# Performance work log

Hardware: AMD Instinct MI355X
Metric: run time of the kernel (lower is better)

Reference implementation:

```python
import jax, jax.numpy as jnp
import numpy as np

NUM_HEADS = 8


def _conv1(x, w, b):
    # 1x1x1 Conv3d == per-voxel channel linear map. x: [B,C,D,H,W], w: [O,C], b: [O]
    return jnp.einsum('bcdhw,oc->bodhw', x, w) + b[None, :, None, None, None]


def setup_inputs() -> dict:
    key = jax.random.key(0)
    ks = jax.random.split(key, 7)
    B, C, D, H, W = 1, 64, 16, 16, 16
    s = 0.02
    return {
        'decoder_features': jax.random.normal(ks[0], (B, C, D, H, W), jnp.float32),
        'mae_features': jax.random.normal(ks[1], (B, C, D, H, W), jnp.float32),
        'q_w': jax.random.normal(ks[2], (C, C), jnp.float32) * s,
        'q_b': jnp.zeros((C,), jnp.float32),
        'k_w': jax.random.normal(ks[3], (C, C), jnp.float32) * s,
        'k_b': jnp.zeros((C,), jnp.float32),
        'v_w': jax.random.normal(ks[4], (C, C), jnp.float32) * s,
        'v_b': jnp.zeros((C,), jnp.float32),
        'o_w': jax.random.normal(ks[5], (C, C), jnp.float32) * s,
        'o_b': jnp.zeros((C,), jnp.float32),
    }


def reference(decoder_features, mae_features, q_w, q_b, k_w, k_b, v_w, v_b, o_w, o_b):
    B, C, D, H, W = decoder_features.shape
    nh = NUM_HEADS
    hd = C // nh
    N = D * H * W
    scale = hd ** -0.5

    def split_heads(x):
        # [B,C,D,H,W] -> [B, nh, N, hd]
        return x.reshape(B, nh, hd, N).transpose(0, 1, 3, 2)

    Q = split_heads(_conv1(decoder_features, q_w, q_b))
    K = split_heads(_conv1(mae_features, k_w, k_b))
    V = split_heads(_conv1(mae_features, v_w, v_b))

    attn = jax.nn.softmax(jnp.einsum('bhnc,bhmc->bhnm', Q, K) * scale, axis=-1)
    out = jnp.einsum('bhnm,bhmc->bhnc', attn, V)  # [B, nh, N, hd]
    out = out.transpose(0, 1, 3, 2).reshape(B, C, D, H, W)
    return _conv1(out, o_w, o_b)
```

## Files before the change

kernel.cpp:

```cpp
#include <hip/hip_runtime.h>
#include <hip/hip_bf16.h>
#include <math.h>


#define N_VOX 4096
#define NH 8
#define QSCALE 0.51010813f

typedef unsigned short ushort_t;
typedef __attribute__((ext_vector_type(8))) short bf16x8;
typedef __attribute__((ext_vector_type(16))) float f32x16;

__device__ __forceinline__ unsigned short f2bf(float f) {
  union { float f; unsigned u; } v; v.f = f;
  unsigned r = v.u + 0x7FFFu + ((v.u >> 16) & 1u);
  return (unsigned short)(r >> 16);
}
__device__ __forceinline__ unsigned pk2bf(float a, float b) {
  __hip_bfloat162 h = __float22bfloat162_rn(float2{a, b});
  union { __hip_bfloat162 h; unsigned u; } c; c.h = h;
  return c.u;
}
__device__ __forceinline__ float ex2(float x) { return __builtin_amdgcn_exp2f(x); }

__global__ __launch_bounds__(256) void qkv_pack(
    const float* __restrict__ dec, const float* __restrict__ mae,
    const float* __restrict__ qw, const float* __restrict__ qb_,
    const float* __restrict__ kw, const float* __restrict__ kb,
    const float* __restrict__ vw, const float* __restrict__ vb,
    ushort_t* __restrict__ Qp, ushort_t* __restrict__ Kp,
    ushort_t* __restrict__ Vt, ushort_t* __restrict__ zeroblk) {
  const int bx = blockIdx.x;
  const int n = blockIdx.y * 256 + threadIdx.x;

  if (bx < 8) {
    const int h = bx;
    float x[64];
#pragma unroll
    for (int c = 0; c < 64; ++c) x[c] = dec[c * N_VOX + n];
    float qv[8];
#pragma unroll
    for (int j = 0; j < 8; ++j) {
      const int o = h * 8 + j;
      float a = qb_[o];
#pragma unroll
      for (int c = 0; c < 64; ++c) a = fmaf(x[c], qw[o * 64 + c], a);
      qv[j] = a * QSCALE;
    }
    uint4 pk;
    pk.x = pk2bf(qv[0], qv[1]); pk.y = pk2bf(qv[2], qv[3]);
    pk.z = pk2bf(qv[4], qv[5]); pk.w = pk2bf(qv[6], qv[7]);
    *(uint4*)(Qp + ((size_t)h * N_VOX + n) * 8) = pk;
  } else {
    const int h = bx - 8;
    float x[64];
#pragma unroll
    for (int c = 0; c < 64; ++c) x[c] = mae[c * N_VOX + n];
    float kv[8], vv[8];
#pragma unroll
    for (int j = 0; j < 8; ++j) {
      const int o = h * 8 + j;
      float a = kb[o], b = vb[o];
#pragma unroll
      for (int c = 0; c < 64; ++c) {
        a = fmaf(x[c], kw[o * 64 + c], a);
        b = fmaf(x[c], vw[o * 64 + c], b);
      }
      kv[j] = a; vv[j] = b;
    }
    uint4 pk;
    pk.x = pk2bf(kv[0], kv[1]); pk.y = pk2bf(kv[2], kv[3]);
    pk.z = pk2bf(kv[4], kv[5]); pk.w = pk2bf(kv[6], kv[7]);
    *(uint4*)(Kp + ((size_t)h * N_VOX + n) * 8) = pk;
#pragma unroll
    for (int d = 0; d < 8; ++d)
      Vt[((size_t)(h * 32 + d)) * N_VOX + n] = f2bf(vv[d]);
    Vt[((size_t)(h * 32 + 8)) * N_VOX + n] = 0x3F80;
    if (h == 0 && n < 8) zeroblk[n] = 0;
  }
}

__global__ __launch_bounds__(256, 3) void attn_mfma(
    const ushort_t* __restrict__ Qp, const ushort_t* __restrict__ Kp,
    const ushort_t* __restrict__ Vt, const ushort_t* __restrict__ zeroblk,
    float* __restrict__ o_part, int kps) {
  const int tid = threadIdx.x;
  const int lane = tid & 63;
  const int wave = tid >> 6;
  const int l31 = lane & 31;
  const int lhalf = lane >> 5;
  const int h = blockIdx.y;
  const int ks = blockIdx.z;
  const int qb = blockIdx.x * 256 + wave * 64;

  __shared__ ushort_t P_lds[8][32 * 36];

  bf16x8 qfrag0 = *(const bf16x8*)(Qp + ((size_t)h * N_VOX + qb + l31) * 8);
  bf16x8 qfrag1 = *(const bf16x8*)(Qp + ((size_t)h * N_VOX + qb + 32 + l31) * 8);

  f32x16 zf, acc0, acc1;
#pragma unroll
  for (int i = 0; i < 16; ++i) { zf[i] = 0.f; acc0[i] = 0.f; acc1[i] = 0.f; }

  const ushort_t* KpH = Kp + (size_t)h * N_VOX * 8;
  const ushort_t* VtH = Vt + ((size_t)h * 32 + l31) * N_VOX;
  ushort_t* pb0 = &P_lds[wave * 2 + 0][l31 * 36];
  ushort_t* pb1 = &P_lds[wave * 2 + 1][l31 * 36];

  const int kbeg = ks * kps;
  for (int kk = 0; kk < kps; kk += 32) {
    const int kcur = kbeg + kk;
    const ushort_t* kp = lhalf ? zeroblk : (KpH + (size_t)(kcur + l31) * 8);
    bf16x8 kf = *(const bf16x8*)kp;

    f32x16 s0 = __builtin_amdgcn_mfma_f32_32x32x16_bf16(kf, qfrag0, zf, 0, 0, 0);
    f32x16 s1 = __builtin_amdgcn_mfma_f32_32x32x16_bf16(kf, qfrag1, zf, 0, 0, 0);

    bf16x8 vf0 = *(const bf16x8*)(VtH + kcur + lhalf * 8);
    bf16x8 vf1 = *(const bf16x8*)(VtH + kcur + 16 + lhalf * 8);

#pragma unroll
    for (int G = 0; G < 4; ++G) {
      uint2 w;
      w.x = pk2bf(ex2(s0[G * 4 + 0]), ex2(s0[G * 4 + 1]));
      w.y = pk2bf(ex2(s0[G * 4 + 2]), ex2(s0[G * 4 + 3]));
      *(uint2*)(pb0 + G * 8 + lhalf * 4) = w;
    }
#pragma unroll
    for (int G = 0; G < 4; ++G) {
      uint2 w;
      w.x = pk2bf(ex2(s1[G * 4 + 0]), ex2(s1[G * 4 + 1]));
      w.y = pk2bf(ex2(s1[G * 4 + 2]), ex2(s1[G * 4 + 3]));
      *(uint2*)(pb1 + G * 8 + lhalf * 4) = w;
    }

#pragma unroll
    for (int grp = 0; grp < 2; ++grp) {
      union { bf16x8 v; uint2 u[2]; } p0, p1;
      p0.u[0] = *(const uint2*)(pb0 + grp * 16 + lhalf * 8);
      p0.u[1] = *(const uint2*)(pb0 + grp * 16 + lhalf * 8 + 4);
      p1.u[0] = *(const uint2*)(pb1 + grp * 16 + lhalf * 8);
      p1.u[1] = *(const uint2*)(pb1 + grp * 16 + lhalf * 8 + 4);
      const bf16x8 vf = grp ? vf1 : vf0;
      acc0 = __builtin_amdgcn_mfma_f32_32x32x16_bf16(p0.v, vf, acc0, 0, 0, 0);
      acc1 = __builtin_amdgcn_mfma_f32_32x32x16_bf16(p1.v, vf, acc1, 0, 0, 0);
    }
  }

  if (l31 < 9) {
    float* ob = o_part + ((size_t)(ks * NH + h) * 9 + l31) * N_VOX;
#pragma unroll
    for (int t = 0; t < 2; ++t) {
      const f32x16 a = t ? acc1 : acc0;
      const int qst = qb + t * 32 + 4 * lhalf;
#pragma unroll
      for (int G = 0; G < 4; ++G) {
        float4 v4 = make_float4(a[G * 4 + 0], a[G * 4 + 1], a[G * 4 + 2], a[G * 4 + 3]);
        *(float4*)(ob + qst + 8 * G) = v4;
      }
    }
  }
}

__global__ __launch_bounds__(256) void combine(
    const float* __restrict__ o_part, float* __restrict__ ocomb, int KS) {
  const int t = blockIdx.x * 256 + threadIdx.x;
  const int c = t >> 12, n = t & (N_VOX - 1);
  const int h = c >> 3, d = c & 7;
  float so = 0.f, sl = 0.f;
  for (int s = 0; s < KS; ++s) {
    const float* base = o_part + ((size_t)(s * NH + h) * 9) * N_VOX;
    so += base[d * N_VOX + n];
    sl += base[8 * N_VOX + n];
  }
  ocomb[(size_t)c * N_VOX + n] = so / sl;
}

__global__ __launch_bounds__(256) void out_proj(
    const float* __restrict__ ocomb, const float* __restrict__ ow,
    const float* __restrict__ obias, float* __restrict__ out) {
  const int og = blockIdx.x;
  const int n = blockIdx.y * 256 + threadIdx.x;
  float x[64];
#pragma unroll
  for (int c = 0; c < 64; ++c) x[c] = ocomb[c * N_VOX + n];
#pragma unroll
  for (int j = 0; j < 8; ++j) {
    const int o = og * 8 + j;
    float acc = obias[o];
#pragma unroll
    for (int c = 0; c < 64; ++c) acc = fmaf(x[c], ow[o * 64 + c], acc);
    out[o * N_VOX + n] = acc;
  }
}

extern "C" void kernel_launch(void* const* d_in, const int* in_sizes, int n_in,
                              void* d_out, int out_size, void* d_ws, size_t ws_size,
                              hipStream_t stream) {
  const float* dec = (const float*)d_in[0];
  const float* mae = (const float*)d_in[1];
  const float* qw = (const float*)d_in[2];
  const float* qb = (const float*)d_in[3];
  const float* kw = (const float*)d_in[4];
  const float* kb = (const float*)d_in[5];
  const float* vw = (const float*)d_in[6];
  const float* vb = (const float*)d_in[7];
  const float* ow = (const float*)d_in[8];
  const float* ob = (const float*)d_in[9];
  float* out = (float*)d_out;
  char* ws = (char*)d_ws;

  const size_t OFF_QP = 0;
  const size_t OFF_KP = 0x80000;
  const size_t OFF_ZERO = 0x100000;
  const size_t OFF_VT = 0x101000;
  const size_t OFF_OPART = 0x301000;

  int KS = 8;
  while (KS > 1) {
    size_t need = OFF_OPART + (size_t)KS * NH * 9 * N_VOX * 4 + 64ull * N_VOX * 4;
    if (need <= ws_size) break;
    KS >>= 1;
  }
  const size_t OFF_OCOMB = OFF_OPART + (size_t)KS * NH * 9 * N_VOX * 4;

  ushort_t* Qp = (ushort_t*)(ws + OFF_QP);
  ushort_t* Kp = (ushort_t*)(ws + OFF_KP);
  ushort_t* zb = (ushort_t*)(ws + OFF_ZERO);
  ushort_t* Vt = (ushort_t*)(ws + OFF_VT);
  float* o_part = (float*)(ws + OFF_OPART);
  float* ocomb = (float*)(ws + OFF_OCOMB);

  qkv_pack<<<dim3(16, 16), 256, 0, stream>>>(dec, mae, qw, qb, kw, kb, vw, vb,
                                             Qp, Kp, Vt, zb);
  attn_mfma<<<dim3(16, 8, KS), 256, 0, stream>>>(Qp, Kp, Vt, zb, o_part,
                                                 N_VOX / KS);
  combine<<<1024, 256, 0, stream>>>(o_part, ocomb, KS);
  out_proj<<<dim3(8, 16), 256, 0, stream>>>(ocomb, ow, ob, out);
}
```

Before: 132.9 us.

## Pack V into MFMA fragment layout, prefetch K/V, raise split-K and occupancy

V is now written in a tiled layout where each lane's 8-element fragment for a 16-key chunk is contiguous, so the attention loop loads V with one coalesced 16-byte read per lane instead of strided rows. K and V fragments for the next iteration are loaded before the current MFMAs, software-pipelining global loads with compute. Split-K is raised from 8 to 16 and launch bounds ask for 4 blocks per SM for more parallelism. The cost is more partial outputs for the combine kernel to read, and more register pressure from the prefetch buffers.

```diff
diff --git a/kernel.cpp b/kernel.cpp
--- a/kernel.cpp
+++ b/kernel.cpp
@@ -29,7 +29,7 @@
     const float* __restrict__ kw, const float* __restrict__ kb,
     const float* __restrict__ vw, const float* __restrict__ vb,
     ushort_t* __restrict__ Qp, ushort_t* __restrict__ Kp,
-    ushort_t* __restrict__ Vt, ushort_t* __restrict__ zeroblk) {
+    ushort_t* __restrict__ VtP, ushort_t* __restrict__ zeroblk) {
   const int bx = blockIdx.x;
   const int n = blockIdx.y * 256 + threadIdx.x;
 
@@ -72,17 +72,20 @@
     pk.x = pk2bf(kv[0], kv[1]); pk.y = pk2bf(kv[2], kv[3]);
     pk.z = pk2bf(kv[4], kv[5]); pk.w = pk2bf(kv[6], kv[7]);
     *(uint4*)(Kp + ((size_t)h * N_VOX + n) * 8) = pk;
-#pragma unroll
-    for (int d = 0; d < 8; ++d)
-      Vt[((size_t)(h * 32 + d)) * N_VOX + n] = f2bf(vv[d]);
-    Vt[((size_t)(h * 32 + 8)) * N_VOX + n] = 0x3F80;
+
+    const size_t base =
+        (((size_t)h * (N_VOX / 16) + (n >> 4)) * 64 + ((n >> 3) & 1) * 32) * 8 +
+        (n & 7);
+#pragma unroll
+    for (int d = 0; d < 8; ++d) VtP[base + (size_t)d * 8] = f2bf(vv[d]);
+    VtP[base + 8 * 8] = 0x3F80;
     if (h == 0 && n < 8) zeroblk[n] = 0;
   }
 }
 
-__global__ __launch_bounds__(256, 3) void attn_mfma(
+__global__ __launch_bounds__(256, 4) void attn_mfma(
     const ushort_t* __restrict__ Qp, const ushort_t* __restrict__ Kp,
-    const ushort_t* __restrict__ Vt, const ushort_t* __restrict__ zeroblk,
+    const ushort_t* __restrict__ VtP, const ushort_t* __restrict__ zeroblk,
     float* __restrict__ o_part, int kps) {
   const int tid = threadIdx.x;
   const int lane = tid & 63;
@@ -103,21 +106,27 @@
   for (int i = 0; i < 16; ++i) { zf[i] = 0.f; acc0[i] = 0.f; acc1[i] = 0.f; }
 
   const ushort_t* KpH = Kp + (size_t)h * N_VOX * 8;
-  const ushort_t* VtH = Vt + ((size_t)h * 32 + l31) * N_VOX;
+  const ushort_t* VtPH = VtP + (size_t)h * (N_VOX / 16) * 64 * 8;
   ushort_t* pb0 = &P_lds[wave * 2 + 0][l31 * 36];
   ushort_t* pb1 = &P_lds[wave * 2 + 1][l31 * 36];
 
   const int kbeg = ks * kps;
+  const ushort_t* kzero = zeroblk;
+
+  bf16x8 kf = *(const bf16x8*)(lhalf ? kzero
+                                     : (KpH + (size_t)(kbeg + l31) * 8));
+  bf16x8 vf0 = *(const bf16x8*)(VtPH + ((size_t)((kbeg >> 4) + 0) * 64 + lane) * 8);
+  bf16x8 vf1 = *(const bf16x8*)(VtPH + ((size_t)((kbeg >> 4) + 1) * 64 + lane) * 8);
+
   for (int kk = 0; kk < kps; kk += 32) {
-    const int kcur = kbeg + kk;
-    const ushort_t* kp = lhalf ? zeroblk : (KpH + (size_t)(kcur + l31) * 8);
-    bf16x8 kf = *(const bf16x8*)kp;
+    const int knext = (kk + 32 < kps) ? (kbeg + kk + 32) : (kbeg + kk);
+    bf16x8 kf_n = *(const bf16x8*)(lhalf ? kzero
+                                         : (KpH + (size_t)(knext + l31) * 8));
+    bf16x8 vf0_n = *(const bf16x8*)(VtPH + ((size_t)((knext >> 4) + 0) * 64 + lane) * 8);
+    bf16x8 vf1_n = *(const bf16x8*)(VtPH + ((size_t)((knext >> 4) + 1) * 64 + lane) * 8);
 
     f32x16 s0 = __builtin_amdgcn_mfma_f32_32x32x16_bf16(kf, qfrag0, zf, 0, 0, 0);
     f32x16 s1 = __builtin_amdgcn_mfma_f32_32x32x16_bf16(kf, qfrag1, zf, 0, 0, 0);
-
-    bf16x8 vf0 = *(const bf16x8*)(VtH + kcur + lhalf * 8);
-    bf16x8 vf1 = *(const bf16x8*)(VtH + kcur + 16 + lhalf * 8);
 
 #pragma unroll
     for (int G = 0; G < 4; ++G) {
@@ -145,6 +154,8 @@
       acc0 = __builtin_amdgcn_mfma_f32_32x32x16_bf16(p0.v, vf, acc0, 0, 0, 0);
       acc1 = __builtin_amdgcn_mfma_f32_32x32x16_bf16(p1.v, vf, acc1, 0, 0, 0);
     }
+
+    kf = kf_n; vf0 = vf0_n; vf1 = vf1_n;
   }
 
   if (l31 < 9) {
@@ -216,7 +227,7 @@
   const size_t OFF_VT = 0x101000;
   const size_t OFF_OPART = 0x301000;
 
-  int KS = 8;
+  int KS = 16;
   while (KS > 1) {
     size_t need = OFF_OPART + (size_t)KS * NH * 9 * N_VOX * 4 + 64ull * N_VOX * 4;
     if (need <= ws_size) break;
@@ -227,13 +238,13 @@
   ushort_t* Qp = (ushort_t*)(ws + OFF_QP);
   ushort_t* Kp = (ushort_t*)(ws + OFF_KP);
   ushort_t* zb = (ushort_t*)(ws + OFF_ZERO);
-  ushort_t* Vt = (ushort_t*)(ws + OFF_VT);
+  ushort_t* VtP = (ushort_t*)(ws + OFF_VT);
   float* o_part = (float*)(ws + OFF_OPART);
   float* ocomb = (float*)(ws + OFF_OCOMB);
 
   qkv_pack<<<dim3(16, 16), 256, 0, stream>>>(dec, mae, qw, qb, kw, kb, vw, vb,
-                                             Qp, Kp, Vt, zb);
-  attn_mfma<<<dim3(16, 8, KS), 256, 0, stream>>>(Qp, Kp, Vt, zb, o_part,
+                                             Qp, Kp, VtP, zb);
+  attn_mfma<<<dim3(16, 8, KS), 256, 0, stream>>>(Qp, Kp, VtP, zb, o_part,
                                                  N_VOX / KS);
   combine<<<1024, 256, 0, stream>>>(o_part, ocomb, KS);
   out_proj<<<dim3(8, 16), 256, 0, stream>>>(ocomb, ow, ob, out);
```

Result: slower. 137.0 us (+3.1%).
